# Performance work log

Measured on AMD Instinct MI355X. Metric: run time of the kernel, lower is better.

## Reference

```python
import jax, jax.numpy as jnp
import numpy as np

B, T, C = 2, 1024, 1024
E, F, K = 8, 2048, 2


def setup_inputs() -> dict:
    key = jax.random.key(0)
    ks = jax.random.split(key, 5)
    s = 1.0 / np.sqrt(C)
    return {
        "x": jax.random.normal(ks[0], (B, T, C), jnp.float32),
        "Wr": jax.random.normal(ks[1], (E, C), jnp.float32) * s,   # router weight [E, d_model]
        "w1": jax.random.normal(ks[2], (E, C, F), jnp.float32) * s, # gate proj per expert
        "w3": jax.random.normal(ks[3], (E, C, F), jnp.float32) * s, # up proj per expert
        "w2": jax.random.normal(ks[4], (E, F, C), jnp.float32) * (1.0 / np.sqrt(F)),  # down proj
    }


def reference(x, Wr, w1, w3, w2):
    Bq, Tq, Cq = x.shape
    flat = x.reshape(-1, Cq)                          # [N, C]
    N = flat.shape[0]
    probs = jax.nn.softmax(flat @ Wr.T, axis=-1)      # [N, E]
    topw, topi = jax.lax.top_k(probs, K)              # [N, K]
    topw = topw / jnp.sum(topw, axis=-1, keepdims=True)
    # dense gate matrix: zero for unselected experts (same math as masked loop)
    gates = jnp.zeros((N, E), flat.dtype).at[jnp.arange(N)[:, None], topi].set(topw)
    # evaluate all experts, weight by gates (gate=0 kills unrouted experts)
    h1 = jnp.einsum('nd,edf->nef', flat, w1)          # [N, E, F]
    h3 = jnp.einsum('nd,edf->nef', flat, w3)
    h = jax.nn.silu(h1) * h3
    y = jnp.einsum('nef,efd->ned', h, w2)             # [N, E, C]
    out = jnp.einsum('ned,ne->nd', y, gates)          # [N, C]
    return out.reshape(Bq, Tq, Cq)
```

## Files before the change

### kernel.cpp

```cpp
#include <hip/hip_runtime.h>
#include <math.h>

typedef _Float16 f16;
typedef _Float16 f16x2 __attribute__((ext_vector_type(2)));
typedef _Float16 f16x4 __attribute__((ext_vector_type(4)));
typedef _Float16 f16x8 __attribute__((ext_vector_type(8)));
typedef __fp16 h16x2 __attribute__((ext_vector_type(2)));
typedef float f32x4 __attribute__((ext_vector_type(4)));

#define N_TOK 2048
#define C_DIM 1024
#define E_NUM 8
#define F_DIM 2048
#define BM 256
#define MAXT2 24

#define WS_COUNTS    0
#define WS_OFFSETS   64
#define WS_TILESTART 128
#define WS_CURSOR    192
#define WS_TOPI      256
#define WS_TOPW      (WS_TOPI + 16384)
#define WS_ROWS      (WS_TOPW + 16384)
#define WS_SLOT      (WS_ROWS + 16384)
#define WS_X16       (1u << 20)
#define WS_H         (6u << 20)
#define WS_Y0        (23u << 20)
#define WS_Y1        (32u << 20)

__device__ __forceinline__ void glds16(const void* g, void* l) {
  __builtin_amdgcn_global_load_lds((const __attribute__((address_space(1))) void*)g,
                                   (__attribute__((address_space(3))) void*)l, 16, 0, 0);
}

__device__ __forceinline__ f16x2 pkrtz(float a, float b) {
  union { h16x2 h; f16x2 f; } u;
  u.h = __builtin_amdgcn_cvt_pkrtz(a, b);
  return u.f;
}

__global__ void cvtx_kernel(const float* __restrict__ x, f16* __restrict__ x16) {
  int i = (blockIdx.x * 256 + threadIdx.x) * 8;
  f32x4 a = *(const f32x4*)(x + i);
  f32x4 b = *(const f32x4*)(x + i + 4);
  union { f16x8 v; f16x2 h[4]; } u;
  u.h[0] = pkrtz(a[0], a[1]);
  u.h[1] = pkrtz(a[2], a[3]);
  u.h[2] = pkrtz(b[0], b[1]);
  u.h[3] = pkrtz(b[2], b[3]);
  *(f16x8*)(x16 + i) = u.v;
}

__global__ void router_kernel(const float* __restrict__ x, const float* __restrict__ Wr,
                              int* counts, int* topi, float* topw) {
  int tok = blockIdx.x * 4 + (threadIdx.x >> 6);
  int lane = threadIdx.x & 63;
  const float* xr = x + (size_t)tok * C_DIM;
  float xv[16];
#pragma unroll
  for (int i = 0; i < 16; ++i) xv[i] = xr[i * 64 + lane];
  float logit[E_NUM];
#pragma unroll
  for (int e = 0; e < E_NUM; ++e) {
    const float* wr = Wr + (size_t)e * C_DIM;
    float acc = 0.f;
#pragma unroll
    for (int i = 0; i < 16; ++i) acc += xv[i] * wr[i * 64 + lane];
#pragma unroll
    for (int s = 1; s < 64; s <<= 1) acc += __shfl_xor(acc, s, 64);
    logit[e] = acc;
  }
  if (lane == 0) {
    float m = logit[0];
#pragma unroll
    for (int e = 1; e < E_NUM; ++e) m = fmaxf(m, logit[e]);
    float p[E_NUM];
#pragma unroll
    for (int e = 0; e < E_NUM; ++e) p[e] = expf(logit[e] - m);
    float p0 = -1.f, p1 = -1.f;
    int i0 = 0, i1 = 0;
#pragma unroll
    for (int e = 0; e < E_NUM; ++e) {
      float v = p[e];
      if (v > p0) { p1 = p0; i1 = i0; p0 = v; i0 = e; }
      else if (v > p1) { p1 = v; i1 = e; }
    }
    float inv = 1.f / (p0 + p1);
    topi[2 * tok] = i0; topi[2 * tok + 1] = i1;
    topw[2 * tok] = p0 * inv; topw[2 * tok + 1] = p1 * inv;
    atomicAdd(&counts[i0], 1);
    atomicAdd(&counts[i1], 1);
  }
}

__global__ void scan_kernel(const int* counts, int* offsets, int* tilestart, int* cursor) {
  if (threadIdx.x == 0) {
    int o = 0, t = 0;
    for (int e = 0; e < E_NUM; ++e) {
      offsets[e] = o; tilestart[e] = t; cursor[e] = o;
      o += counts[e];
      t += (counts[e] + 255) >> 8;
    }
    offsets[E_NUM] = o; tilestart[E_NUM] = t;
  }
}

__global__ void scatter_kernel(const int* __restrict__ topi, int* cursor,
                               int* rows_perm, int* slot_of) {
  int n = blockIdx.x * blockDim.x + threadIdx.x;
  if (n >= N_TOK) return;
#pragma unroll
  for (int k = 0; k < 2; ++k) {
    int e = topi[2 * n + k];
    int pos = atomicAdd(&cursor[e], 1);
    rows_perm[pos] = n;
    slot_of[2 * n + k] = pos;
  }
}

__launch_bounds__(512, 2)
__global__ void upproj_kernel(const f16* __restrict__ x16,
                              const float* __restrict__ w1,
                              const float* __restrict__ w3,
                              const int* __restrict__ counts,
                              const int* __restrict__ offsets,
                              const int* __restrict__ tilestart,
                              const int* __restrict__ rows_perm,
                              f16* __restrict__ h_buf) {
  __shared__ f16 A_lds[2][BM * 32];
  __shared__ f16 B1_lds[2][128 * 32];
  __shared__ f16 B3_lds[2][128 * 32];

  int rt = blockIdx.y;
  int e = -1;
#pragma unroll
  for (int i = 0; i < E_NUM; ++i)
    if (rt >= tilestart[i] && rt < tilestart[i + 1]) e = i;
  if (e < 0) return;
  int row0 = (rt - tilestart[e]) * BM;
  int cnt = counts[e], off = offsets[e];
  int f0 = blockIdx.x * 128;
  int t = threadIdx.x, wid = t >> 6, lane = t & 63;

  const f16* asrc[2];
#pragma unroll
  for (int p = 0; p < 2; ++p) {
    int c = (p * 8 + wid) * 64 + lane;
    int row = c >> 2, cc = c & 3;
    int lr = row0 + row; if (lr > cnt - 1) lr = cnt - 1;
    int g = rows_perm[off + lr];
    asrc[p] = x16 + (size_t)g * C_DIM + 8 * (cc ^ ((row >> 1) & 3));
  }

  int bcol = t & 127, kg = t >> 7;
  int bso = bcol * 32 + (kg ^ ((bcol >> 1) & 3)) * 8;
  const size_t eb = (size_t)e * C_DIM * F_DIM;
  const float* w1p = w1 + eb + (size_t)(kg * 8) * F_DIM + f0 + bcol;
  const float* w3p = w3 + eb + (size_t)(kg * 8) * F_DIM + f0 + bcol;

  f32x4 acc1[4][4] = {};
  f32x4 acc3[4][4] = {};
  int wr = (wid >> 1) * 64, wc = (wid & 1) * 64;
  int fr = lane & 15, fq = lane >> 4;

  float r1[8], r3[8];
#pragma unroll
  for (int j = 0; j < 8; ++j) {
    r1[j] = w1p[(size_t)j * F_DIM];
    r3[j] = w3p[(size_t)j * F_DIM];
  }
  glds16(asrc[0], &A_lds[0][wid * 512]);
  glds16(asrc[1], &A_lds[0][(8 + wid) * 512]);

#pragma unroll 2
  for (int tt = 0; tt < 32; ++tt) {
    int cur = tt & 1;
    {
      union { f16x8 v; f16x2 h[4]; } u;
      u.h[0] = pkrtz(r1[0], r1[1]); u.h[1] = pkrtz(r1[2], r1[3]);
      u.h[2] = pkrtz(r1[4], r1[5]); u.h[3] = pkrtz(r1[6], r1[7]);
      *(f16x8*)&B1_lds[cur][bso] = u.v;
      u.h[0] = pkrtz(r3[0], r3[1]); u.h[1] = pkrtz(r3[2], r3[3]);
      u.h[2] = pkrtz(r3[4], r3[5]); u.h[3] = pkrtz(r3[6], r3[7]);
      *(f16x8*)&B3_lds[cur][bso] = u.v;
    }
    __syncthreads();
    int knext = ((tt + 1) & 31) * 32;
    glds16(asrc[0] + knext, &A_lds[cur ^ 1][wid * 512]);
    glds16(asrc[1] + knext, &A_lds[cur ^ 1][(8 + wid) * 512]);
#pragma unroll
    for (int j = 0; j < 8; ++j) {
      r1[j] = w1p[(size_t)(knext + j) * F_DIM];
      r3[j] = w3p[(size_t)(knext + j) * F_DIM];
    }
    f16x8 a[4];
#pragma unroll
    for (int m = 0; m < 4; ++m) {
      int row = wr + m * 16 + fr;
      a[m] = *(const f16x8*)&A_lds[cur][row * 32 + (fq ^ ((row >> 1) & 3)) * 8];
    }
    f16x8 b[4];
#pragma unroll
    for (int n = 0; n < 4; ++n) {
      int col = wc + n * 16 + fr;
      b[n] = *(const f16x8*)&B1_lds[cur][col * 32 + (fq ^ ((col >> 1) & 3)) * 8];
    }
#pragma unroll
    for (int m = 0; m < 4; ++m)
#pragma unroll
      for (int n = 0; n < 4; ++n)
        acc1[m][n] = __builtin_amdgcn_mfma_f32_16x16x32_f16(a[m], b[n], acc1[m][n], 0, 0, 0);
#pragma unroll
    for (int n = 0; n < 4; ++n) {
      int col = wc + n * 16 + fr;
      b[n] = *(const f16x8*)&B3_lds[cur][col * 32 + (fq ^ ((col >> 1) & 3)) * 8];
    }
#pragma unroll
    for (int m = 0; m < 4; ++m)
#pragma unroll
      for (int n = 0; n < 4; ++n)
        acc3[m][n] = __builtin_amdgcn_mfma_f32_16x16x32_f16(a[m], b[n], acc3[m][n], 0, 0, 0);
  }

#pragma unroll
  for (int m = 0; m < 4; ++m)
#pragma unroll
    for (int n = 0; n < 4; ++n)
#pragma unroll
      for (int i = 0; i < 4; ++i) {
        int lr = row0 + wr + m * 16 + fq * 4 + i;
        if (lr < cnt) {
          float v1 = acc1[m][n][i], v3 = acc3[m][n][i];
          float hval = v1 / (1.f + expf(-v1)) * v3;
          h_buf[(size_t)(off + lr) * F_DIM + f0 + wc + n * 16 + fr] = (f16)hval;
        }
      }
}

__launch_bounds__(512, 2)
__global__ void downproj_kernel(const f16* __restrict__ h_buf,
                                const float* __restrict__ w2,
                                const int* __restrict__ counts,
                                const int* __restrict__ offsets,
                                const int* __restrict__ tilestart,
                                f16* __restrict__ y0,
                                f16* __restrict__ y1) {
  __shared__ f16 A_lds[2][BM * 32];
  __shared__ f16 B_lds[2][128 * 32];

  int kh = blockIdx.z;
  f16* yb = kh ? y1 : y0;
  int rt = blockIdx.y;
  int e = -1;
#pragma unroll
  for (int i = 0; i < E_NUM; ++i)
    if (rt >= tilestart[i] && rt < tilestart[i + 1]) e = i;
  if (e < 0) return;
  int row0 = (rt - tilestart[e]) * BM;
  int cnt = counts[e], off = offsets[e];
  int c0 = blockIdx.x * 128;
  int t = threadIdx.x, wid = t >> 6, lane = t & 63;

  const f16* asrc[2];
#pragma unroll
  for (int p = 0; p < 2; ++p) {
    int c = (p * 8 + wid) * 64 + lane;
    int row = c >> 2, cc = c & 3;
    int lr = row0 + row; if (lr > cnt - 1) lr = cnt - 1;
    asrc[p] = h_buf + (size_t)(off + lr) * F_DIM + kh * 1024 + 8 * (cc ^ ((row >> 1) & 3));
  }

  int bcol = t & 127, kg = t >> 7;
  int bso = bcol * 32 + (kg ^ ((bcol >> 1) & 3)) * 8;
  const float* w2p = w2 + (size_t)e * F_DIM * C_DIM
                     + (size_t)(kh * 1024 + kg * 8) * C_DIM + c0 + bcol;

  f32x4 acc[4][4] = {};
  int wr = (wid >> 1) * 64, wc = (wid & 1) * 64;
  int fr = lane & 15, fq = lane >> 4;

  float rb[8];
#pragma unroll
  for (int j = 0; j < 8; ++j) rb[j] = w2p[(size_t)j * C_DIM];
  glds16(asrc[0], &A_lds[0][wid * 512]);
  glds16(asrc[1], &A_lds[0][(8 + wid) * 512]);

#pragma unroll 2
  for (int tt = 0; tt < 32; ++tt) {
    int cur = tt & 1;
    {
      union { f16x8 v; f16x2 h[4]; } u;
      u.h[0] = pkrtz(rb[0], rb[1]); u.h[1] = pkrtz(rb[2], rb[3]);
      u.h[2] = pkrtz(rb[4], rb[5]); u.h[3] = pkrtz(rb[6], rb[7]);
      *(f16x8*)&B_lds[cur][bso] = u.v;
    }
    __syncthreads();
    int knext = ((tt + 1) & 31) * 32;
    glds16(asrc[0] + knext, &A_lds[cur ^ 1][wid * 512]);
    glds16(asrc[1] + knext, &A_lds[cur ^ 1][(8 + wid) * 512]);
#pragma unroll
    for (int j = 0; j < 8; ++j) rb[j] = w2p[(size_t)(knext + j) * C_DIM];
    f16x8 a[4];
#pragma unroll
    for (int m = 0; m < 4; ++m) {
      int row = wr + m * 16 + fr;
      a[m] = *(const f16x8*)&A_lds[cur][row * 32 + (fq ^ ((row >> 1) & 3)) * 8];
    }
    f16x8 b[4];
#pragma unroll
    for (int n = 0; n < 4; ++n) {
      int col = wc + n * 16 + fr;
      b[n] = *(const f16x8*)&B_lds[cur][col * 32 + (fq ^ ((col >> 1) & 3)) * 8];
    }
#pragma unroll
    for (int m = 0; m < 4; ++m)
#pragma unroll
      for (int n = 0; n < 4; ++n)
        acc[m][n] = __builtin_amdgcn_mfma_f32_16x16x32_f16(a[m], b[n], acc[m][n], 0, 0, 0);
  }

#pragma unroll
  for (int m = 0; m < 4; ++m)
#pragma unroll
    for (int n = 0; n < 4; ++n)
#pragma unroll
      for (int i = 0; i < 4; ++i) {
        int lr = row0 + wr + m * 16 + fq * 4 + i;
        if (lr < cnt)
          yb[(size_t)(off + lr) * C_DIM + c0 + wc + n * 16 + fr] = (f16)acc[m][n][i];
      }
}

__global__ void combine_kernel(const f16* __restrict__ y0, const f16* __restrict__ y1,
                               const int* __restrict__ slot_of,
                               const float* __restrict__ topw,
                               float* __restrict__ out) {
  int n = blockIdx.x;
  int s0 = slot_of[2 * n], s1 = slot_of[2 * n + 1];
  float g0 = topw[2 * n], g1 = topw[2 * n + 1];
  int c = threadIdx.x * 4;
  f16x4 a0 = *(const f16x4*)(y0 + (size_t)s0 * C_DIM + c);
  f16x4 a1 = *(const f16x4*)(y1 + (size_t)s0 * C_DIM + c);
  f16x4 b0 = *(const f16x4*)(y0 + (size_t)s1 * C_DIM + c);
  f16x4 b1 = *(const f16x4*)(y1 + (size_t)s1 * C_DIM + c);
  f32x4 o;
#pragma unroll
  for (int i = 0; i < 4; ++i)
    o[i] = g0 * ((float)a0[i] + (float)a1[i]) + g1 * ((float)b0[i] + (float)b1[i]);
  *(f32x4*)(out + (size_t)n * C_DIM + c) = o;
}

extern "C" void kernel_launch(void* const* d_in, const int* in_sizes, int n_in,
                              void* d_out, int out_size, void* d_ws, size_t ws_size,
                              hipStream_t stream) {
  const float* x  = (const float*)d_in[0];
  const float* Wr = (const float*)d_in[1];
  const float* w1 = (const float*)d_in[2];
  const float* w3 = (const float*)d_in[3];
  const float* w2 = (const float*)d_in[4];
  float* out = (float*)d_out;
  char* ws = (char*)d_ws;

  int* counts    = (int*)(ws + WS_COUNTS);
  int* offsets   = (int*)(ws + WS_OFFSETS);
  int* tilestart = (int*)(ws + WS_TILESTART);
  int* cursor    = (int*)(ws + WS_CURSOR);
  int* topi      = (int*)(ws + WS_TOPI);
  float* topw    = (float*)(ws + WS_TOPW);
  int* rows_perm = (int*)(ws + WS_ROWS);
  int* slot_of   = (int*)(ws + WS_SLOT);
  f16* x16       = (f16*)(ws + WS_X16);
  f16* h_buf     = (f16*)(ws + WS_H);
  f16* y0        = (f16*)(ws + WS_Y0);
  f16* y1        = (f16*)(ws + WS_Y1);

  (void)hipMemsetAsync(ws, 0, 256, stream);
  cvtx_kernel<<<N_TOK * C_DIM / 8 / 256, 256, 0, stream>>>(x, x16);
  router_kernel<<<N_TOK / 4, 256, 0, stream>>>(x, Wr, counts, topi, topw);
  scan_kernel<<<1, 64, 0, stream>>>(counts, offsets, tilestart, cursor);
  scatter_kernel<<<N_TOK / 256, 256, 0, stream>>>(topi, cursor, rows_perm, slot_of);
  upproj_kernel<<<dim3(F_DIM / 128, MAXT2), 512, 0, stream>>>(
      x16, w1, w3, counts, offsets, tilestart, rows_perm, h_buf);
  downproj_kernel<<<dim3(C_DIM / 128, MAXT2, 2), 512, 0, stream>>>(
      h_buf, w2, counts, offsets, tilestart, y0, y1);
  combine_kernel<<<N_TOK, 256, 0, stream>>>(y0, y1, slot_of, topw, out);
}
```

Baseline: 215.0 us.

## Triple-buffer A tiles with fine-grained waits and expert-interleaved block mapping

Both expert GEMM kernels now keep three A-tile buffers in LDS and two register sets of prefetched weights. Each step uses an explicit lgkmcnt wait, a raw barrier and a partial vmcnt wait, so loads run two k-steps ahead instead of one, aiming to hide global load latency. The launch grid becomes 1D with the expert index in the low bits, so concurrent blocks spread over experts, and the tilestart prefix scan is dropped. Idle tiles exit early, which allows up to 8 tiles per expert. The hand-written vmcnt counts are fragile and rely on the compiler emitting loads in the expected order. The extra A buffer also raises LDS use per block.

```diff
diff --git a/kernel.cpp b/kernel.cpp
--- a/kernel.cpp
+++ b/kernel.cpp
@@ -13,11 +13,9 @@
 #define E_NUM 8
 #define F_DIM 2048
 #define BM 256
-#define MAXT2 24
 
 #define WS_COUNTS    0
 #define WS_OFFSETS   64
-#define WS_TILESTART 128
 #define WS_CURSOR    192
 #define WS_TOPI      256
 #define WS_TOPW      (WS_TOPI + 16384)
@@ -93,15 +91,14 @@
   }
 }
 
-__global__ void scan_kernel(const int* counts, int* offsets, int* tilestart, int* cursor) {
+__global__ void scan_kernel(const int* counts, int* offsets, int* cursor) {
   if (threadIdx.x == 0) {
-    int o = 0, t = 0;
+    int o = 0;
     for (int e = 0; e < E_NUM; ++e) {
-      offsets[e] = o; tilestart[e] = t; cursor[e] = o;
+      offsets[e] = o; cursor[e] = o;
       o += counts[e];
-      t += (counts[e] + 255) >> 8;
     }
-    offsets[E_NUM] = o; tilestart[E_NUM] = t;
+    offsets[E_NUM] = o;
   }
 }
 
@@ -117,6 +114,44 @@
     slot_of[2 * n + k] = pos;
   }
 }
+
+#define UP_STEP(R1, R3)                                                          \
+  do {                                                                           \
+    { union { f16x8 v; f16x2 h[4]; } u;                                          \
+      u.h[0] = pkrtz(R1[0], R1[1]); u.h[1] = pkrtz(R1[2], R1[3]);                \
+      u.h[2] = pkrtz(R1[4], R1[5]); u.h[3] = pkrtz(R1[6], R1[7]);                \
+      *(f16x8*)&B1_lds[cur][bso] = u.v;                                          \
+      u.h[0] = pkrtz(R3[0], R3[1]); u.h[1] = pkrtz(R3[2], R3[3]);                \
+      u.h[2] = pkrtz(R3[4], R3[5]); u.h[3] = pkrtz(R3[6], R3[7]);                \
+      *(f16x8*)&B3_lds[cur][bso] = u.v; }                                        \
+    asm volatile("s_waitcnt lgkmcnt(0)" ::: "memory");                           \
+    __builtin_amdgcn_s_barrier();                                                \
+    { int kn = ((ti + 2) & 31) * 32;                                             \
+      _Pragma("unroll") for (int j = 0; j < 8; ++j) {                            \
+        R1[j] = w1p[(size_t)(kn + j) * F_DIM];                                   \
+        R3[j] = w3p[(size_t)(kn + j) * F_DIM]; }                                 \
+      glds16(asrc[0] + kn, a_wr + wid * 512);                                    \
+      glds16(asrc[1] + kn, a_wr + (8 + wid) * 512); }                            \
+    asm volatile("s_waitcnt vmcnt(36)" ::: "memory");                            \
+    { f16x8 a[4], b[4];                                                          \
+      _Pragma("unroll") for (int m = 0; m < 4; ++m) {                            \
+        int row = wr + m * 16 + fr;                                              \
+        a[m] = *(const f16x8*)&a_rd0[row * 32 + (fq ^ ((row >> 1) & 3)) * 8]; }  \
+      _Pragma("unroll") for (int n = 0; n < 4; ++n) {                            \
+        int col = wc + n * 16 + fr;                                              \
+        b[n] = *(const f16x8*)&B1_lds[cur][col * 32 + (fq ^ ((col >> 1) & 3)) * 8]; } \
+      _Pragma("unroll") for (int m = 0; m < 4; ++m)                              \
+        _Pragma("unroll") for (int n = 0; n < 4; ++n)                            \
+          acc1[m][n] = __builtin_amdgcn_mfma_f32_16x16x32_f16(a[m], b[n], acc1[m][n], 0, 0, 0); \
+      _Pragma("unroll") for (int n = 0; n < 4; ++n) {                            \
+        int col = wc + n * 16 + fr;                                              \
+        b[n] = *(const f16x8*)&B3_lds[cur][col * 32 + (fq ^ ((col >> 1) & 3)) * 8]; } \
+      _Pragma("unroll") for (int m = 0; m < 4; ++m)                              \
+        _Pragma("unroll") for (int n = 0; n < 4; ++n)                            \
+          acc3[m][n] = __builtin_amdgcn_mfma_f32_16x16x32_f16(a[m], b[n], acc3[m][n], 0, 0, 0); } \
+    { f16* _t = a_rd0; a_rd0 = a_rd1; a_rd1 = a_wr; a_wr = _t; }                 \
+    ++ti; cur ^= 1;                                                              \
+  } while (0)
 
 __launch_bounds__(512, 2)
 __global__ void upproj_kernel(const f16* __restrict__ x16,
@@ -124,22 +159,22 @@
                               const float* __restrict__ w3,
                               const int* __restrict__ counts,
                               const int* __restrict__ offsets,
-                              const int* __restrict__ tilestart,
                               const int* __restrict__ rows_perm,
                               f16* __restrict__ h_buf) {
-  __shared__ f16 A_lds[2][BM * 32];
+  __shared__ f16 A_lds[3][BM * 32];
   __shared__ f16 B1_lds[2][128 * 32];
   __shared__ f16 B3_lds[2][128 * 32];
 
-  int rt = blockIdx.y;
-  int e = -1;
-#pragma unroll
-  for (int i = 0; i < E_NUM; ++i)
-    if (rt >= tilestart[i] && rt < tilestart[i + 1]) e = i;
-  if (e < 0) return;
-  int row0 = (rt - tilestart[e]) * BM;
-  int cnt = counts[e], off = offsets[e];
-  int f0 = blockIdx.x * 128;
+  int bid = blockIdx.x;
+  int e = bid & 7;
+  int slot = bid >> 3;
+  int tile = slot >> 4;
+  int fidx = slot & 15;
+  int cnt = counts[e];
+  if (tile * BM >= cnt) return;
+  int row0 = tile * BM;
+  int off = offsets[e];
+  int f0 = fidx * 128;
   int t = threadIdx.x, wid = t >> 6, lane = t & 63;
 
   const f16* asrc[2];
@@ -163,63 +198,24 @@
   int wr = (wid >> 1) * 64, wc = (wid & 1) * 64;
   int fr = lane & 15, fq = lane >> 4;
 
-  float r1[8], r3[8];
-#pragma unroll
-  for (int j = 0; j < 8; ++j) {
-    r1[j] = w1p[(size_t)j * F_DIM];
-    r3[j] = w3p[(size_t)j * F_DIM];
-  }
-  glds16(asrc[0], &A_lds[0][wid * 512]);
-  glds16(asrc[1], &A_lds[0][(8 + wid) * 512]);
-
-#pragma unroll 2
-  for (int tt = 0; tt < 32; ++tt) {
-    int cur = tt & 1;
-    {
-      union { f16x8 v; f16x2 h[4]; } u;
-      u.h[0] = pkrtz(r1[0], r1[1]); u.h[1] = pkrtz(r1[2], r1[3]);
-      u.h[2] = pkrtz(r1[4], r1[5]); u.h[3] = pkrtz(r1[6], r1[7]);
-      *(f16x8*)&B1_lds[cur][bso] = u.v;
-      u.h[0] = pkrtz(r3[0], r3[1]); u.h[1] = pkrtz(r3[2], r3[3]);
-      u.h[2] = pkrtz(r3[4], r3[5]); u.h[3] = pkrtz(r3[6], r3[7]);
-      *(f16x8*)&B3_lds[cur][bso] = u.v;
-    }
-    __syncthreads();
-    int knext = ((tt + 1) & 31) * 32;
-    glds16(asrc[0] + knext, &A_lds[cur ^ 1][wid * 512]);
-    glds16(asrc[1] + knext, &A_lds[cur ^ 1][(8 + wid) * 512]);
-#pragma unroll
-    for (int j = 0; j < 8; ++j) {
-      r1[j] = w1p[(size_t)(knext + j) * F_DIM];
-      r3[j] = w3p[(size_t)(knext + j) * F_DIM];
-    }
-    f16x8 a[4];
-#pragma unroll
-    for (int m = 0; m < 4; ++m) {
-      int row = wr + m * 16 + fr;
-      a[m] = *(const f16x8*)&A_lds[cur][row * 32 + (fq ^ ((row >> 1) & 3)) * 8];
-    }
-    f16x8 b[4];
-#pragma unroll
-    for (int n = 0; n < 4; ++n) {
-      int col = wc + n * 16 + fr;
-      b[n] = *(const f16x8*)&B1_lds[cur][col * 32 + (fq ^ ((col >> 1) & 3)) * 8];
-    }
-#pragma unroll
-    for (int m = 0; m < 4; ++m)
-#pragma unroll
-      for (int n = 0; n < 4; ++n)
-        acc1[m][n] = __builtin_amdgcn_mfma_f32_16x16x32_f16(a[m], b[n], acc1[m][n], 0, 0, 0);
-#pragma unroll
-    for (int n = 0; n < 4; ++n) {
-      int col = wc + n * 16 + fr;
-      b[n] = *(const f16x8*)&B3_lds[cur][col * 32 + (fq ^ ((col >> 1) & 3)) * 8];
-    }
-#pragma unroll
-    for (int m = 0; m < 4; ++m)
-#pragma unroll
-      for (int n = 0; n < 4; ++n)
-        acc3[m][n] = __builtin_amdgcn_mfma_f32_16x16x32_f16(a[m], b[n], acc3[m][n], 0, 0, 0);
+  f16* a_rd0 = &A_lds[0][0];
+  f16* a_rd1 = &A_lds[1][0];
+  f16* a_wr  = &A_lds[2][0];
+
+  float rA1[8], rA3[8], rB1[8], rB3[8];
+#pragma unroll
+  for (int j = 0; j < 8; ++j) { rA1[j] = w1p[(size_t)j * F_DIM]; rA3[j] = w3p[(size_t)j * F_DIM]; }
+  glds16(asrc[0], a_rd0 + wid * 512);
+  glds16(asrc[1], a_rd0 + (8 + wid) * 512);
+#pragma unroll
+  for (int j = 0; j < 8; ++j) { rB1[j] = w1p[(size_t)(32 + j) * F_DIM]; rB3[j] = w3p[(size_t)(32 + j) * F_DIM]; }
+  glds16(asrc[0] + 32, a_rd1 + wid * 512);
+  glds16(asrc[1] + 32, a_rd1 + (8 + wid) * 512);
+
+  int ti = 0, cur = 0;
+  for (int tp = 0; tp < 16; ++tp) {
+    UP_STEP(rA1, rA3);
+    UP_STEP(rB1, rB3);
   }
 
 #pragma unroll
@@ -237,28 +233,56 @@
       }
 }
 
+#define DN_STEP(RB)                                                              \
+  do {                                                                           \
+    { union { f16x8 v; f16x2 h[4]; } u;                                          \
+      u.h[0] = pkrtz(RB[0], RB[1]); u.h[1] = pkrtz(RB[2], RB[3]);                \
+      u.h[2] = pkrtz(RB[4], RB[5]); u.h[3] = pkrtz(RB[6], RB[7]);                \
+      *(f16x8*)&B_lds[cur][bso] = u.v; }                                         \
+    asm volatile("s_waitcnt lgkmcnt(0)" ::: "memory");                           \
+    __builtin_amdgcn_s_barrier();                                                \
+    { int kn = ((ti + 2) & 31) * 32;                                             \
+      _Pragma("unroll") for (int j = 0; j < 8; ++j)                              \
+        RB[j] = w2p[(size_t)(kn + j) * C_DIM];                                   \
+      glds16(asrc[0] + kn, a_wr + wid * 512);                                    \
+      glds16(asrc[1] + kn, a_wr + (8 + wid) * 512); }                            \
+    asm volatile("s_waitcnt vmcnt(20)" ::: "memory");                            \
+    { f16x8 a[4], b[4];                                                          \
+      _Pragma("unroll") for (int m = 0; m < 4; ++m) {                            \
+        int row = wr + m * 16 + fr;                                              \
+        a[m] = *(const f16x8*)&a_rd0[row * 32 + (fq ^ ((row >> 1) & 3)) * 8]; }  \
+      _Pragma("unroll") for (int n = 0; n < 4; ++n) {                            \
+        int col = wc + n * 16 + fr;                                              \
+        b[n] = *(const f16x8*)&B_lds[cur][col * 32 + (fq ^ ((col >> 1) & 3)) * 8]; } \
+      _Pragma("unroll") for (int m = 0; m < 4; ++m)                              \
+        _Pragma("unroll") for (int n = 0; n < 4; ++n)                            \
+          acc[m][n] = __builtin_amdgcn_mfma_f32_16x16x32_f16(a[m], b[n], acc[m][n], 0, 0, 0); } \
+    { f16* _t = a_rd0; a_rd0 = a_rd1; a_rd1 = a_wr; a_wr = _t; }                 \
+    ++ti; cur ^= 1;                                                              \
+  } while (0)
+
 __launch_bounds__(512, 2)
 __global__ void downproj_kernel(const f16* __restrict__ h_buf,
                                 const float* __restrict__ w2,
                                 const int* __restrict__ counts,
                                 const int* __restrict__ offsets,
-                                const int* __restrict__ tilestart,
                                 f16* __restrict__ y0,
                                 f16* __restrict__ y1) {
-  __shared__ f16 A_lds[2][BM * 32];
+  __shared__ f16 A_lds[3][BM * 32];
   __shared__ f16 B_lds[2][128 * 32];
 
-  int kh = blockIdx.z;
+  int bid = blockIdx.x;
+  int e = bid & 7;
+  int slot = bid >> 3;
+  int kh = slot & 1;
+  int tile = (slot >> 1) & 7;
+  int cidx = slot >> 4;
+  int cnt = counts[e];
+  if (tile * BM >= cnt) return;
   f16* yb = kh ? y1 : y0;
-  int rt = blockIdx.y;
-  int e = -1;
-#pragma unroll
-  for (int i = 0; i < E_NUM; ++i)
-    if (rt >= tilestart[i] && rt < tilestart[i + 1]) e = i;
-  if (e < 0) return;
-  int row0 = (rt - tilestart[e]) * BM;
-  int cnt = counts[e], off = offsets[e];
-  int c0 = blockIdx.x * 128;
+  int row0 = tile * BM;
+  int off = offsets[e];
+  int c0 = cidx * 128;
   int t = threadIdx.x, wid = t >> 6, lane = t & 63;
 
   const f16* asrc[2];
@@ -279,44 +303,24 @@
   int wr = (wid >> 1) * 64, wc = (wid & 1) * 64;
   int fr = lane & 15, fq = lane >> 4;
 
-  float rb[8];
-#pragma unroll
-  for (int j = 0; j < 8; ++j) rb[j] = w2p[(size_t)j * C_DIM];
-  glds16(asrc[0], &A_lds[0][wid * 512]);
-  glds16(asrc[1], &A_lds[0][(8 + wid) * 512]);
-
-#pragma unroll 2
-  for (int tt = 0; tt < 32; ++tt) {
-    int cur = tt & 1;
-    {
-      union { f16x8 v; f16x2 h[4]; } u;
-      u.h[0] = pkrtz(rb[0], rb[1]); u.h[1] = pkrtz(rb[2], rb[3]);
-      u.h[2] = pkrtz(rb[4], rb[5]); u.h[3] = pkrtz(rb[6], rb[7]);
-      *(f16x8*)&B_lds[cur][bso] = u.v;
-    }
-    __syncthreads();
-    int knext = ((tt + 1) & 31) * 32;
-    glds16(asrc[0] + knext, &A_lds[cur ^ 1][wid * 512]);
-    glds16(asrc[1] + knext, &A_lds[cur ^ 1][(8 + wid) * 512]);
-#pragma unroll
-    for (int j = 0; j < 8; ++j) rb[j] = w2p[(size_t)(knext + j) * C_DIM];
-    f16x8 a[4];
-#pragma unroll
-    for (int m = 0; m < 4; ++m) {
-      int row = wr + m * 16 + fr;
-      a[m] = *(const f16x8*)&A_lds[cur][row * 32 + (fq ^ ((row >> 1) & 3)) * 8];
-    }
-    f16x8 b[4];
-#pragma unroll
-    for (int n = 0; n < 4; ++n) {
-      int col = wc + n * 16 + fr;
-      b[n] = *(const f16x8*)&B_lds[cur][col * 32 + (fq ^ ((col >> 1) & 3)) * 8];
-    }
-#pragma unroll
-    for (int m = 0; m < 4; ++m)
-#pragma unroll
-      for (int n = 0; n < 4; ++n)
-        acc[m][n] = __builtin_amdgcn_mfma_f32_16x16x32_f16(a[m], b[n], acc[m][n], 0, 0, 0);
+  f16* a_rd0 = &A_lds[0][0];
+  f16* a_rd1 = &A_lds[1][0];
+  f16* a_wr  = &A_lds[2][0];
+
+  float rA[8], rB[8];
+#pragma unroll
+  for (int j = 0; j < 8; ++j) rA[j] = w2p[(size_t)j * C_DIM];
+  glds16(asrc[0], a_rd0 + wid * 512);
+  glds16(asrc[1], a_rd0 + (8 + wid) * 512);
+#pragma unroll
+  for (int j = 0; j < 8; ++j) rB[j] = w2p[(size_t)(32 + j) * C_DIM];
+  glds16(asrc[0] + 32, a_rd1 + wid * 512);
+  glds16(asrc[1] + 32, a_rd1 + (8 + wid) * 512);
+
+  int ti = 0, cur = 0;
+  for (int tp = 0; tp < 16; ++tp) {
+    DN_STEP(rA);
+    DN_STEP(rB);
   }
 
 #pragma unroll
@@ -363,7 +367,6 @@
 
   int* counts    = (int*)(ws + WS_COUNTS);
   int* offsets   = (int*)(ws + WS_OFFSETS);
-  int* tilestart = (int*)(ws + WS_TILESTART);
   int* cursor    = (int*)(ws + WS_CURSOR);
   int* topi      = (int*)(ws + WS_TOPI);
   float* topw    = (float*)(ws + WS_TOPW);
@@ -377,11 +380,11 @@
   (void)hipMemsetAsync(ws, 0, 256, stream);
   cvtx_kernel<<<N_TOK * C_DIM / 8 / 256, 256, 0, stream>>>(x, x16);
   router_kernel<<<N_TOK / 4, 256, 0, stream>>>(x, Wr, counts, topi, topw);
-  scan_kernel<<<1, 64, 0, stream>>>(counts, offsets, tilestart, cursor);
+  scan_kernel<<<1, 64, 0, stream>>>(counts, offsets, cursor);
   scatter_kernel<<<N_TOK / 256, 256, 0, stream>>>(topi, cursor, rows_perm, slot_of);
-  upproj_kernel<<<dim3(F_DIM / 128, MAXT2), 512, 0, stream>>>(
-      x16, w1, w3, counts, offsets, tilestart, rows_perm, h_buf);
-  downproj_kernel<<<dim3(C_DIM / 128, MAXT2, 2), 512, 0, stream>>>(
-      h_buf, w2, counts, offsets, tilestart, y0, y1);
+  upproj_kernel<<<E_NUM * 128, 512, 0, stream>>>(
+      x16, w1, w3, counts, offsets, rows_perm, h_buf);
+  downproj_kernel<<<E_NUM * 128, 512, 0, stream>>>(
+      h_buf, w2, counts, offsets, y0, y1);
   combine_kernel<<<N_TOK, 256, 0, stream>>>(y0, y1, slot_of, topw, out);
 }
```

New measurement: 216.2 us. Within noise of the previous version (+0.6%).
